# Optimization experiments

Hardware: AMD Instinct MI355X
Metric: run time of the kernel (lower is better)

The kernel has to match this reference:

```python
import jax, jax.numpy as jnp
import numpy as np

H = 8        # num_heads
D = 64       # qkv_dim
E = 512      # embed_dim = H*D
MS = 16      # ms_hidden_dim


def setup_inputs() -> dict:
    key = jax.random.key(0)
    ks = jax.random.split(key, 12)
    b, r, c = 4, 512, 512
    row_emb = jax.random.normal(ks[0], (b, r, E), dtype=jnp.float32)
    col_emb = jax.random.normal(ks[1], (b, c, E), dtype=jnp.float32)
    cost_mat = jax.random.uniform(ks[2], (b, r, c), dtype=jnp.float32)
    attn_mask = jax.random.randint(ks[3], (b, H, r, c), 0, 2) > 0
    s = 1.0 / np.sqrt(E)
    Wq = jax.random.uniform(ks[4], (H * D, E), minval=-s, maxval=s)
    Wk = jax.random.uniform(ks[5], (H * D, E), minval=-s, maxval=s)
    Wv = jax.random.uniform(ks[6], (H * D, E), minval=-s, maxval=s)
    Wout = jax.random.uniform(ks[7], (E, E), minval=-s, maxval=s)
    m1 = np.sqrt(0.5)
    m2 = np.sqrt(1.0 / MS)
    Wmix1 = jax.random.uniform(ks[8], (H * MS, 2 * H), minval=-m1, maxval=m1)
    Wmix2 = jax.random.uniform(ks[9], (H, H * MS), minval=-m2, maxval=m2)
    return {"row_emb": row_emb, "col_emb": col_emb, "cost_mat": cost_mat,
            "attn_mask": attn_mask, "Wq": Wq, "Wk": Wk, "Wv": Wv,
            "Wmix1": Wmix1, "Wmix2": Wmix2, "Wout": Wout}


def reference(row_emb, col_emb, cost_mat, attn_mask, Wq, Wk, Wv, Wmix1, Wmix2, Wout):
    b, r, _ = row_emb.shape
    c = col_emb.shape[1]
    norm = 1.0 / jnp.sqrt(jnp.asarray(D, row_emb.dtype))
    # projections -> [b, h, s, d]
    q = (row_emb @ Wq.T).reshape(b, r, H, D).transpose(0, 2, 1, 3)
    k = (col_emb @ Wk.T).reshape(b, c, H, D).transpose(0, 2, 1, 3)
    v = (col_emb @ Wv.T).reshape(b, c, H, D).transpose(0, 2, 1, 3)
    dot = norm * jnp.einsum('bhrd,bhcd->bhrc', q, k)            # [b,h,r,c]
    cost = jnp.broadcast_to(cost_mat[:, None, :, :], dot.shape)  # [b,h,r,c]
    # stack then rearrange 'b h r c s -> b r c (h s)' (h major, s minor)
    two = jnp.stack([dot, cost], axis=-1)                        # [b,h,r,c,2]
    two = two.transpose(0, 2, 3, 1, 4).reshape(b, r, c, 2 * H)
    hid = jax.nn.relu(two @ Wmix1.T)                             # [b,r,c,H*MS]
    ms = hid @ Wmix2.T                                           # [b,r,c,H]
    logits = ms.transpose(0, 3, 1, 2)                            # [b,h,r,c]
    # mask handling: rows that are fully masked become fully unmasked
    all_masked = jnp.all(attn_mask, axis=-1, keepdims=True)
    mask = jnp.where(all_masked, False, attn_mask)
    logits = jnp.where(mask, -jnp.inf, logits)
    weights = jax.nn.softmax(logits, axis=-1)
    out = jnp.einsum('bhrc,bhcd->bhrd', weights, v)              # [b,h,r,d]
    out = out.transpose(0, 2, 1, 3).reshape(b, r, H * D)         # b s (h d)
    return out @ Wout.T
```

## Files before the change

kernel.cpp:

```cpp
#include <hip/hip_runtime.h>
#include <math.h>

typedef __attribute__((ext_vector_type(8))) short bf16x8;
typedef __attribute__((ext_vector_type(4))) float f32x4;
typedef unsigned short ushort_t;

static __device__ inline unsigned short f2bf(float f) {
    union { float f; unsigned u; } v; v.f = f;
    unsigned r = v.u + 0x7fff + ((v.u >> 16) & 1);
    return (unsigned short)(r >> 16);
}

#if defined(__has_builtin)
#  if __has_builtin(__builtin_amdgcn_cvt_pk_bf16_f32)
#    define HAVE_PK_BF16 1
#  endif
#endif

static __device__ inline unsigned pk2bf(float a, float b) {
#ifdef HAVE_PK_BF16
    auto r = __builtin_amdgcn_cvt_pk_bf16_f32(a, b);
    unsigned u; __builtin_memcpy(&u, &r, 4);
    return u;
#else
    return (unsigned)f2bf(a) | ((unsigned)f2bf(b) << 16);
#endif
}

__global__ __launch_bounds__(256) void convert_all(const float* __restrict__ a0,
                                                   const float* __restrict__ a1,
                                                   const float* __restrict__ a2,
                                                   const float* __restrict__ a3,
                                                   const float* __restrict__ a4,
                                                   const float* __restrict__ a5,
                                                   ushort_t* __restrict__ dst) {
    const size_t e = ((size_t)blockIdx.x * 256 + threadIdx.x) * 4;
    const float* src; size_t off;
    if      (e < 1048576) { src = a0; off = 0; }
    else if (e < 2097152) { src = a1; off = 1048576; }
    else if (e < 2359296) { src = a2; off = 2097152; }
    else if (e < 2621440) { src = a3; off = 2359296; }
    else if (e < 2883584) { src = a4; off = 2621440; }
    else                  { src = a5; off = 2883584; }
    const float4 v = *(const float4*)(src + (e - off));
    uint2 o; o.x = pk2bf(v.x, v.y); o.y = pk2bf(v.z, v.w);
    *(uint2*)(dst + e) = o;
}

__global__ __launch_bounds__(256) void gemm_qkv(const ushort_t* __restrict__ rowb,
                                                const ushort_t* __restrict__ colb,
                                                const ushort_t* __restrict__ Wqb,
                                                const ushort_t* __restrict__ Wkb,
                                                const ushort_t* __restrict__ Wvb,
                                                ushort_t* __restrict__ Qb,
                                                ushort_t* __restrict__ Kb,
                                                ushort_t* __restrict__ Vt) {
    const int z = blockIdx.z;
    const ushort_t* A = (z == 0) ? rowb : colb;
    const ushort_t* B = (z == 0) ? Wqb : (z == 1) ? Wkb : Wvb;

    const int t    = threadIdx.x;
    const int w    = t >> 6;
    const int lane = t & 63;
    const int quad = lane >> 4;
    const int sl   = lane & 15;
    const int m0 = blockIdx.x * 64 + (w >> 1) * 32;
    const int n0 = blockIdx.y * 64 + (w & 1) * 32;

    const ushort_t* ap0 = A + (size_t)(m0 + sl) * 512 + quad * 8;
    const ushort_t* ap1 = A + (size_t)(m0 + 16 + sl) * 512 + quad * 8;
    const ushort_t* bp0 = B + (size_t)(n0 + sl) * 512 + quad * 8;
    const ushort_t* bp1 = B + (size_t)(n0 + 16 + sl) * 512 + quad * 8;

    f32x4 acc[2][2] = {};

    bf16x8 a0 = *(const bf16x8*)ap0;
    bf16x8 a1 = *(const bf16x8*)ap1;
    bf16x8 b0 = *(const bf16x8*)bp0;
    bf16x8 b1 = *(const bf16x8*)bp1;

    for (int ks = 0; ks < 16; ++ks) {
        bf16x8 na0, na1, nb0, nb1;
        if (ks < 15) {
            const int k0 = (ks + 1) * 32;
            na0 = *(const bf16x8*)(ap0 + k0);
            na1 = *(const bf16x8*)(ap1 + k0);
            nb0 = *(const bf16x8*)(bp0 + k0);
            nb1 = *(const bf16x8*)(bp1 + k0);
        }
        acc[0][0] = __builtin_amdgcn_mfma_f32_16x16x32_bf16(a0, b0, acc[0][0], 0, 0, 0);
        acc[0][1] = __builtin_amdgcn_mfma_f32_16x16x32_bf16(a0, b1, acc[0][1], 0, 0, 0);
        acc[1][0] = __builtin_amdgcn_mfma_f32_16x16x32_bf16(a1, b0, acc[1][0], 0, 0, 0);
        acc[1][1] = __builtin_amdgcn_mfma_f32_16x16x32_bf16(a1, b1, acc[1][1], 0, 0, 0);
        a0 = na0; a1 = na1; b0 = nb0; b1 = nb1;
    }

#pragma unroll
    for (int rs = 0; rs < 2; ++rs)
#pragma unroll
        for (int cs = 0; cs < 2; ++cs) {
            const int n = n0 + cs * 16 + sl;
            if (z == 2) {
                const int mb   = m0 + rs * 16 + quad * 4;
                const int bidx = mb >> 9, c = mb & 511;
                const int h = n >> 6, d = n & 63;
                ushort4 o;
                o.x = f2bf(acc[rs][cs][0]); o.y = f2bf(acc[rs][cs][1]);
                o.z = f2bf(acc[rs][cs][2]); o.w = f2bf(acc[rs][cs][3]);
                *(ushort4*)(Vt + (size_t)(((bidx * 8 + h) * 64 + d)) * 512 + c) = o;
            } else {
                ushort_t* C = (z == 0) ? Qb : Kb;
#pragma unroll
                for (int reg = 0; reg < 4; ++reg) {
                    const int m = m0 + rs * 16 + quad * 4 + reg;
                    C[(size_t)m * 512 + n] = f2bf(acc[rs][cs][reg]);
                }
            }
        }
}

__global__ __launch_bounds__(256) void gemm_out(const ushort_t* __restrict__ A,
                                                const ushort_t* __restrict__ B,
                                                float* __restrict__ C) {
    const int t    = threadIdx.x;
    const int w    = t >> 6;
    const int lane = t & 63;
    const int quad = lane >> 4;
    const int sl   = lane & 15;
    const int m0 = blockIdx.x * 64 + (w >> 1) * 32;
    const int n0 = blockIdx.y * 64 + (w & 1) * 32;

    const ushort_t* ap0 = A + (size_t)(m0 + sl) * 512 + quad * 8;
    const ushort_t* ap1 = A + (size_t)(m0 + 16 + sl) * 512 + quad * 8;
    const ushort_t* bp0 = B + (size_t)(n0 + sl) * 512 + quad * 8;
    const ushort_t* bp1 = B + (size_t)(n0 + 16 + sl) * 512 + quad * 8;

    f32x4 acc[2][2] = {};

    bf16x8 a0 = *(const bf16x8*)ap0;
    bf16x8 a1 = *(const bf16x8*)ap1;
    bf16x8 b0 = *(const bf16x8*)bp0;
    bf16x8 b1 = *(const bf16x8*)bp1;

    for (int ks = 0; ks < 16; ++ks) {
        bf16x8 na0, na1, nb0, nb1;
        if (ks < 15) {
            const int k0 = (ks + 1) * 32;
            na0 = *(const bf16x8*)(ap0 + k0);
            na1 = *(const bf16x8*)(ap1 + k0);
            nb0 = *(const bf16x8*)(bp0 + k0);
            nb1 = *(const bf16x8*)(bp1 + k0);
        }
        acc[0][0] = __builtin_amdgcn_mfma_f32_16x16x32_bf16(a0, b0, acc[0][0], 0, 0, 0);
        acc[0][1] = __builtin_amdgcn_mfma_f32_16x16x32_bf16(a0, b1, acc[0][1], 0, 0, 0);
        acc[1][0] = __builtin_amdgcn_mfma_f32_16x16x32_bf16(a1, b0, acc[1][0], 0, 0, 0);
        acc[1][1] = __builtin_amdgcn_mfma_f32_16x16x32_bf16(a1, b1, acc[1][1], 0, 0, 0);
        a0 = na0; a1 = na1; b0 = nb0; b1 = nb1;
    }

#pragma unroll
    for (int rs = 0; rs < 2; ++rs)
#pragma unroll
        for (int cs = 0; cs < 2; ++cs) {
            const int n = n0 + cs * 16 + sl;
#pragma unroll
            for (int reg = 0; reg < 4; ++reg) {
                const int m = m0 + rs * 16 + quad * 4 + reg;
                C[(size_t)m * 512 + n] = acc[rs][cs][reg];
            }
        }
}

__global__ __launch_bounds__(512) void dot_mlp_v5(const ushort_t* __restrict__ Qb,
                                                  const ushort_t* __restrict__ Kb,
                                                  const float* __restrict__ cost,
                                                  const float* __restrict__ W1,
                                                  const float* __restrict__ W2,
                                                  float* __restrict__ logits) {
    __shared__ ushort_t Xs[1024 * 18];
    __shared__ ushort_t hidS[8 * 16 * 36];
    __shared__ ushort_t W1fs[128 * 16];
    __shared__ ushort_t W2ss[8 * 128];

    const int b  = blockIdx.z;
    const int r0 = blockIdx.y * 32;
    const int c0 = blockIdx.x * 32;
    const int t    = threadIdx.x;
    const int w    = t >> 6;
    const int lane = t & 63;
    const int quad = lane >> 4;
    const int sl   = lane & 15;

    const bf16x8 zf = {0, 0, 0, 0, 0, 0, 0, 0};

    if (t < 128) {
        float s = 0.f;
#pragma unroll
        for (int h = 0; h < 8; ++h) {
            W1fs[t * 16 + h] = f2bf(W1[t * 16 + 2 * h]);
            s += W1[t * 16 + 2 * h + 1];
        }
        W1fs[t * 16 + 8] = f2bf(s);
#pragma unroll
        for (int k = 9; k < 16; ++k) W1fs[t * 16 + k] = 0;
    }
#pragma unroll
    for (int i = 0; i < 2; ++i) W2ss[t + i * 512] = f2bf(W2[t + i * 512]);

#pragma unroll
    for (int i = 0; i < 2; ++i) {
        const int cell = t + i * 512;
        const int rl = cell >> 5, cl = cell & 31;
        unsigned* base = (unsigned*)(Xs + cell * 18 + 8);
        base[0] = (unsigned)f2bf(cost[((size_t)b * 512 + r0 + rl) * 512 + c0 + cl]);
        base[1] = 0; base[2] = 0; base[3] = 0; base[4] = 0;
    }

    {
        const int hp = w & 3;
        const int h0 = hp * 2;
        const int rs = w >> 2;
        bf16x8 af[2][2], bfr[2][2][2];
#pragma unroll
        for (int hh = 0; hh < 2; ++hh)
#pragma unroll
            for (int ks = 0; ks < 2; ++ks) {
                af[hh][ks] = *(const bf16x8*)(Qb +
                    ((size_t)(b * 512 + r0 + rs * 16 + sl) * 512 + (h0 + hh) * 64 + ks * 32 + quad * 8));
#pragma unroll
                for (int cs = 0; cs < 2; ++cs)
                    bfr[hh][cs][ks] = *(const bf16x8*)(Kb +
                        ((size_t)(b * 512 + c0 + cs * 16 + sl) * 512 + (h0 + hh) * 64 + ks * 32 + quad * 8));
            }
        f32x4 dacc[2][2];
#pragma unroll
        for (int hh = 0; hh < 2; ++hh)
#pragma unroll
            for (int cs = 0; cs < 2; ++cs) {
                f32x4 acc = {0.f, 0.f, 0.f, 0.f};
                acc = __builtin_amdgcn_mfma_f32_16x16x32_bf16(af[hh][0], bfr[hh][cs][0], acc, 0, 0, 0);
                acc = __builtin_amdgcn_mfma_f32_16x16x32_bf16(af[hh][1], bfr[hh][cs][1], acc, 0, 0, 0);
                dacc[hh][cs] = acc;
            }
#pragma unroll
        for (int cs = 0; cs < 2; ++cs)
#pragma unroll
            for (int reg = 0; reg < 4; ++reg) {
                const int cell = (rs * 16 + quad * 4 + reg) * 32 + cs * 16 + sl;
                ((unsigned*)Xs)[cell * 9 + hp] =
                    pk2bf(dacc[0][cs][reg] * 0.125f, dacc[1][cs][reg] * 0.125f);
            }
    }

    __syncthreads();

    bf16x8 bw1[8];
#pragma unroll
    for (int nt = 0; nt < 8; ++nt)
        bw1[nt] = (quad < 2) ? *(const bf16x8*)&W1fs[(nt * 16 + sl) * 16 + quad * 8] : zf;
    bf16x8 bw2[4];
#pragma unroll
    for (int ks = 0; ks < 4; ++ks) {
        union { ushort_t s[8]; bf16x8 v; } tu;
#pragma unroll
        for (int i = 0; i < 8; ++i) {
            const int p  = quad * 8 + i;
            const int jc = (p >> 1) | ((p & 1) << 4);
            tu.s[i] = (sl < 8) ? W2ss[sl * 128 + ks * 32 + jc] : (ushort_t)0;
        }
        bw2[ks] = tu.v;
    }

    ushort_t* hidW = hidS + w * (16 * 36);

#pragma unroll
    for (int mt = 0; mt < 8; ++mt) {
        const int gmt = w * 8 + mt;
        const int cb  = gmt * 16;

        bf16x8 a1 = zf;
        if (quad < 2) {
            const unsigned* xr = (const unsigned*)Xs + (size_t)(cb + sl) * 9 + quad * 4;
            union { unsigned u[4]; bf16x8 v; } tmp;
            tmp.u[0] = xr[0]; tmp.u[1] = xr[1]; tmp.u[2] = xr[2]; tmp.u[3] = xr[3];
            a1 = tmp.v;
        }

        f32x4 acc2 = {0.f, 0.f, 0.f, 0.f};
#pragma unroll
        for (int ks = 0; ks < 4; ++ks) {
            f32x4 z = {0.f, 0.f, 0.f, 0.f};
            const f32x4 h0 = __builtin_amdgcn_mfma_f32_16x16x32_bf16(a1, bw1[2 * ks],     z, 0, 0, 0);
            const f32x4 h1 = __builtin_amdgcn_mfma_f32_16x16x32_bf16(a1, bw1[2 * ks + 1], z, 0, 0, 0);
#pragma unroll
            for (int rp = 0; rp < 4; ++rp)
                ((unsigned*)hidW)[(quad * 4 + rp) * 18 + sl] =
                    pk2bf(fmaxf(h0[rp], 0.f), fmaxf(h1[rp], 0.f));
            union { uint2 u2[2]; bf16x8 v; } tu;
            const ushort_t* hp2 = hidW + sl * 36 + quad * 8;
            tu.u2[0] = *(const uint2*)hp2;
            tu.u2[1] = *(const uint2*)(hp2 + 4);
            acc2 = __builtin_amdgcn_mfma_f32_16x16x32_bf16(tu.v, bw2[ks], acc2, 0, 0, 0);
        }

        if (sl < 8) {
            const int r = r0 + (gmt >> 1);
            const int cbase = c0 + (gmt & 1) * 16 + quad * 4;
            float4 o; o.x = acc2[0]; o.y = acc2[1]; o.z = acc2[2]; o.w = acc2[3];
            *(float4*)&logits[((size_t)(b * 8 + sl) * 512 + r) * 512 + cbase] = o;
        }
    }
}

__global__ __launch_bounds__(256) void softmax_pv(const float* __restrict__ logits,
                                                  const int* __restrict__ mask,
                                                  const ushort_t* __restrict__ Vt,
                                                  ushort_t* __restrict__ Aout) {
    __shared__ ushort_t Ps[16 * 520];

    const int t    = threadIdx.x;
    const int w    = t >> 6;
    const int lane = t & 63;
    const int quad = lane >> 4;
    const int sl   = lane & 15;
    const int rt = blockIdx.x;
    const int bh = blockIdx.y;
    const int r0 = rt * 16;

#pragma unroll
    for (int rr = 0; rr < 4; ++rr) {
        const int row = w * 4 + rr;
        const float* lp = logits + ((size_t)bh * 512 + r0 + row) * 512;
        const int*   mp = mask   + ((size_t)bh * 512 + r0 + row) * 512;

        float v[8]; int m[8]; int allm = 1;
#pragma unroll
        for (int i = 0; i < 8; ++i) {
            v[i] = lp[lane + i * 64];
            m[i] = mp[lane + i * 64];
            allm &= (m[i] != 0);
        }
        const bool all_masked = (__all(allm) != 0);

        float mx = -__builtin_inff();
#pragma unroll
        for (int i = 0; i < 8; ++i) {
            const bool keep = all_masked || (m[i] == 0);
            if (keep) mx = fmaxf(mx, v[i]);
        }
#pragma unroll
        for (int s = 32; s > 0; s >>= 1) mx = fmaxf(mx, __shfl_xor(mx, s, 64));

        float e[8]; float sum = 0.f;
#pragma unroll
        for (int i = 0; i < 8; ++i) {
            const bool keep = all_masked || (m[i] == 0);
            e[i] = keep ? __expf(v[i] - mx) : 0.f;
            sum += e[i];
        }
#pragma unroll
        for (int s = 32; s > 0; s >>= 1) sum += __shfl_xor(sum, s, 64);

        const float inv = 1.f / sum;
#pragma unroll
        for (int i = 0; i < 8; ++i)
            Ps[row * 520 + lane + i * 64] = f2bf(e[i] * inv);
    }

    __syncthreads();

    const int n0w = w * 16;
    const ushort_t* vb = Vt + (size_t)bh * 64 * 512;

    f32x4 acc = {0.f, 0.f, 0.f, 0.f};
    for (int ks = 0; ks < 16; ++ks) {
        union { uint2 u2[2]; bf16x8 v; } ta;
        const ushort_t* pp = Ps + (size_t)sl * 520 + ks * 32 + quad * 8;
        ta.u2[0] = *(const uint2*)pp;
        ta.u2[1] = *(const uint2*)(pp + 4);
        const bf16x8 bv = *(const bf16x8*)(vb + (size_t)(n0w + sl) * 512 + ks * 32 + quad * 8);
        acc = __builtin_amdgcn_mfma_f32_16x16x32_bf16(ta.v, bv, acc, 0, 0, 0);
    }

    const int bidx = bh >> 3, h = bh & 7;
    ushort_t* Cb = Aout + (size_t)bidx * 512 * 512 + h * 64;
    const int n = n0w + sl;
#pragma unroll
    for (int reg = 0; reg < 4; ++reg) {
        const int m = r0 + quad * 4 + reg;
        Cb[(size_t)m * 512 + n] = f2bf(acc[reg]);
    }
}

extern "C" void kernel_launch(void* const* d_in, const int* in_sizes, int n_in,
                              void* d_out, int out_size, void* d_ws, size_t ws_size,
                              hipStream_t stream) {
    const float* row_emb = (const float*)d_in[0];
    const float* col_emb = (const float*)d_in[1];
    const float* cost    = (const float*)d_in[2];
    const int*   mask    = (const int*)d_in[3];
    const float* Wq      = (const float*)d_in[4];
    const float* Wk      = (const float*)d_in[5];
    const float* Wv      = (const float*)d_in[6];
    const float* Wmix1   = (const float*)d_in[7];
    const float* Wmix2   = (const float*)d_in[8];
    const float* Wout    = (const float*)d_in[9];
    float* out = (float*)d_out;

    char* ws = (char*)d_ws;
    const size_t MB = (size_t)1 << 20;
    ushort_t* convDst = (ushort_t*)ws;
    ushort_t* rowb  = (ushort_t*)(ws);
    ushort_t* colb  = (ushort_t*)(ws + 2 * MB);
    ushort_t* Wqb   = (ushort_t*)(ws + 4 * MB);
    ushort_t* Wkb   = (ushort_t*)(ws + 4 * MB + 512 * 1024);
    ushort_t* Wvb   = (ushort_t*)(ws + 5 * MB);
    ushort_t* Woutb = (ushort_t*)(ws + 5 * MB + 512 * 1024);
    ushort_t* Qb    = (ushort_t*)(ws + 6 * MB);
    ushort_t* Kb    = (ushort_t*)(ws + 8 * MB);
    ushort_t* Vt    = (ushort_t*)(ws + 10 * MB);
    ushort_t* Aoutb = (ushort_t*)(ws + 12 * MB);
    float* logitsBuf = (float*)(ws + 16 * MB);

    convert_all<<<3072, 256, 0, stream>>>(row_emb, col_emb, Wq, Wk, Wv, Wout, convDst);

    gemm_qkv<<<dim3(32, 8, 3), 256, 0, stream>>>(rowb, colb, Wqb, Wkb, Wvb, Qb, Kb, Vt);

    dot_mlp_v5<<<dim3(16, 16, 4), 512, 0, stream>>>(Qb, Kb, cost, Wmix1, Wmix2, logitsBuf);

    softmax_pv<<<dim3(32, 32), 256, 0, stream>>>(logitsBuf, mask, Vt, Aoutb);

    gemm_out<<<dim3(32, 8), 256, 0, stream>>>(Aoutb, Woutb, out);
}
```

Baseline: 190.6 us.

## Shrink GEMM tiles with split-K accumulators, swizzle X smem, batch hidden MFMAs

The QKV and output GEMMs now use 32-row block tiles and run two independent K-half accumulator chains per wave. This doubles the grid and adds instruction-level parallelism, at the cost of reloading the B operand more often. In the dot/MLP kernel, an XOR row swizzle is applied to the Xs shared tile to cut LDS bank conflicts. All eight first-layer MFMAs are now issued before any hidden values go to a wider, padded shared buffer, which removes the per-step store/load serialization. This raises register and LDS use.

```diff
diff --git a/kernel.cpp b/kernel.cpp
--- a/kernel.cpp
+++ b/kernel.cpp
@@ -25,6 +25,10 @@
 #else
     return (unsigned)f2bf(a) | ((unsigned)f2bf(b) << 16);
 #endif
+}
+
+static __device__ inline int xrow(int cell) {
+    return cell ^ (((cell >> 7) & 1) << 4);
 }
 
 __global__ __launch_bounds__(256) void convert_all(const float* __restrict__ a0,
@@ -64,59 +68,58 @@
     const int lane = t & 63;
     const int quad = lane >> 4;
     const int sl   = lane & 15;
-    const int m0 = blockIdx.x * 64 + (w >> 1) * 32;
+    const int m0 = blockIdx.x * 32 + (w >> 1) * 16;
     const int n0 = blockIdx.y * 64 + (w & 1) * 32;
 
-    const ushort_t* ap0 = A + (size_t)(m0 + sl) * 512 + quad * 8;
-    const ushort_t* ap1 = A + (size_t)(m0 + 16 + sl) * 512 + quad * 8;
+    const ushort_t* ap  = A + (size_t)(m0 + sl) * 512 + quad * 8;
     const ushort_t* bp0 = B + (size_t)(n0 + sl) * 512 + quad * 8;
     const ushort_t* bp1 = B + (size_t)(n0 + 16 + sl) * 512 + quad * 8;
 
-    f32x4 acc[2][2] = {};
-
-    bf16x8 a0 = *(const bf16x8*)ap0;
-    bf16x8 a1 = *(const bf16x8*)ap1;
-    bf16x8 b0 = *(const bf16x8*)bp0;
-    bf16x8 b1 = *(const bf16x8*)bp1;
-
-    for (int ks = 0; ks < 16; ++ks) {
-        bf16x8 na0, na1, nb0, nb1;
-        if (ks < 15) {
-            const int k0 = (ks + 1) * 32;
-            na0 = *(const bf16x8*)(ap0 + k0);
-            na1 = *(const bf16x8*)(ap1 + k0);
-            nb0 = *(const bf16x8*)(bp0 + k0);
-            nb1 = *(const bf16x8*)(bp1 + k0);
-        }
-        acc[0][0] = __builtin_amdgcn_mfma_f32_16x16x32_bf16(a0, b0, acc[0][0], 0, 0, 0);
-        acc[0][1] = __builtin_amdgcn_mfma_f32_16x16x32_bf16(a0, b1, acc[0][1], 0, 0, 0);
-        acc[1][0] = __builtin_amdgcn_mfma_f32_16x16x32_bf16(a1, b0, acc[1][0], 0, 0, 0);
-        acc[1][1] = __builtin_amdgcn_mfma_f32_16x16x32_bf16(a1, b1, acc[1][1], 0, 0, 0);
-        a0 = na0; a1 = na1; b0 = nb0; b1 = nb1;
-    }
-
-#pragma unroll
-    for (int rs = 0; rs < 2; ++rs)
-#pragma unroll
-        for (int cs = 0; cs < 2; ++cs) {
-            const int n = n0 + cs * 16 + sl;
-            if (z == 2) {
-                const int mb   = m0 + rs * 16 + quad * 4;
-                const int bidx = mb >> 9, c = mb & 511;
-                const int h = n >> 6, d = n & 63;
-                ushort4 o;
-                o.x = f2bf(acc[rs][cs][0]); o.y = f2bf(acc[rs][cs][1]);
-                o.z = f2bf(acc[rs][cs][2]); o.w = f2bf(acc[rs][cs][3]);
-                *(ushort4*)(Vt + (size_t)(((bidx * 8 + h) * 64 + d)) * 512 + c) = o;
-            } else {
-                ushort_t* C = (z == 0) ? Qb : Kb;
-#pragma unroll
-                for (int reg = 0; reg < 4; ++reg) {
-                    const int m = m0 + rs * 16 + quad * 4 + reg;
-                    C[(size_t)m * 512 + n] = f2bf(acc[rs][cs][reg]);
-                }
+    f32x4 accA[2] = {}, accB[2] = {};
+
+    bf16x8 aA = *(const bf16x8*)ap,          b0A = *(const bf16x8*)bp0,
+           b1A = *(const bf16x8*)bp1;
+    bf16x8 aB = *(const bf16x8*)(ap + 256),  b0B = *(const bf16x8*)(bp0 + 256),
+           b1B = *(const bf16x8*)(bp1 + 256);
+
+    for (int ks = 0; ks < 8; ++ks) {
+        bf16x8 naA, nb0A, nb1A, naB, nb0B, nb1B;
+        if (ks < 7) {
+            const int o = (ks + 1) * 32;
+            naA  = *(const bf16x8*)(ap + o);        nb0A = *(const bf16x8*)(bp0 + o);
+            nb1A = *(const bf16x8*)(bp1 + o);
+            naB  = *(const bf16x8*)(ap + 256 + o);  nb0B = *(const bf16x8*)(bp0 + 256 + o);
+            nb1B = *(const bf16x8*)(bp1 + 256 + o);
+        }
+        accA[0] = __builtin_amdgcn_mfma_f32_16x16x32_bf16(aA, b0A, accA[0], 0, 0, 0);
+        accA[1] = __builtin_amdgcn_mfma_f32_16x16x32_bf16(aA, b1A, accA[1], 0, 0, 0);
+        accB[0] = __builtin_amdgcn_mfma_f32_16x16x32_bf16(aB, b0B, accB[0], 0, 0, 0);
+        accB[1] = __builtin_amdgcn_mfma_f32_16x16x32_bf16(aB, b1B, accB[1], 0, 0, 0);
+        aA = naA; b0A = nb0A; b1A = nb1A;
+        aB = naB; b0B = nb0B; b1B = nb1B;
+    }
+
+#pragma unroll
+    for (int cs = 0; cs < 2; ++cs) {
+        const f32x4 acc = accA[cs] + accB[cs];
+        const int n = n0 + cs * 16 + sl;
+        if (z == 2) {
+            const int mb   = m0 + quad * 4;
+            const int bidx = mb >> 9, c = mb & 511;
+            const int h = n >> 6, d = n & 63;
+            ushort4 o;
+            o.x = f2bf(acc[0]); o.y = f2bf(acc[1]);
+            o.z = f2bf(acc[2]); o.w = f2bf(acc[3]);
+            *(ushort4*)(Vt + (size_t)(((bidx * 8 + h) * 64 + d)) * 512 + c) = o;
+        } else {
+            ushort_t* C = (z == 0) ? Qb : Kb;
+#pragma unroll
+            for (int reg = 0; reg < 4; ++reg) {
+                const int m = m0 + quad * 4 + reg;
+                C[(size_t)m * 512 + n] = f2bf(acc[reg]);
             }
         }
+    }
 }
 
 __global__ __launch_bounds__(256) void gemm_out(const ushort_t* __restrict__ A,
@@ -127,58 +130,57 @@
     const int lane = t & 63;
     const int quad = lane >> 4;
     const int sl   = lane & 15;
-    const int m0 = blockIdx.x * 64 + (w >> 1) * 32;
+    const int m0 = blockIdx.x * 32 + (w >> 1) * 16;
     const int n0 = blockIdx.y * 64 + (w & 1) * 32;
 
-    const ushort_t* ap0 = A + (size_t)(m0 + sl) * 512 + quad * 8;
-    const ushort_t* ap1 = A + (size_t)(m0 + 16 + sl) * 512 + quad * 8;
+    const ushort_t* ap  = A + (size_t)(m0 + sl) * 512 + quad * 8;
     const ushort_t* bp0 = B + (size_t)(n0 + sl) * 512 + quad * 8;
     const ushort_t* bp1 = B + (size_t)(n0 + 16 + sl) * 512 + quad * 8;
 
-    f32x4 acc[2][2] = {};
-
-    bf16x8 a0 = *(const bf16x8*)ap0;
-    bf16x8 a1 = *(const bf16x8*)ap1;
-    bf16x8 b0 = *(const bf16x8*)bp0;
-    bf16x8 b1 = *(const bf16x8*)bp1;
-
-    for (int ks = 0; ks < 16; ++ks) {
-        bf16x8 na0, na1, nb0, nb1;
-        if (ks < 15) {
-            const int k0 = (ks + 1) * 32;
-            na0 = *(const bf16x8*)(ap0 + k0);
-            na1 = *(const bf16x8*)(ap1 + k0);
-            nb0 = *(const bf16x8*)(bp0 + k0);
-            nb1 = *(const bf16x8*)(bp1 + k0);
-        }
-        acc[0][0] = __builtin_amdgcn_mfma_f32_16x16x32_bf16(a0, b0, acc[0][0], 0, 0, 0);
-        acc[0][1] = __builtin_amdgcn_mfma_f32_16x16x32_bf16(a0, b1, acc[0][1], 0, 0, 0);
-        acc[1][0] = __builtin_amdgcn_mfma_f32_16x16x32_bf16(a1, b0, acc[1][0], 0, 0, 0);
-        acc[1][1] = __builtin_amdgcn_mfma_f32_16x16x32_bf16(a1, b1, acc[1][1], 0, 0, 0);
-        a0 = na0; a1 = na1; b0 = nb0; b1 = nb1;
-    }
-
-#pragma unroll
-    for (int rs = 0; rs < 2; ++rs)
-#pragma unroll
-        for (int cs = 0; cs < 2; ++cs) {
-            const int n = n0 + cs * 16 + sl;
-#pragma unroll
-            for (int reg = 0; reg < 4; ++reg) {
-                const int m = m0 + rs * 16 + quad * 4 + reg;
-                C[(size_t)m * 512 + n] = acc[rs][cs][reg];
-            }
-        }
-}
-
-__global__ __launch_bounds__(512) void dot_mlp_v5(const ushort_t* __restrict__ Qb,
+    f32x4 accA[2] = {}, accB[2] = {};
+
+    bf16x8 aA = *(const bf16x8*)ap,          b0A = *(const bf16x8*)bp0,
+           b1A = *(const bf16x8*)bp1;
+    bf16x8 aB = *(const bf16x8*)(ap + 256),  b0B = *(const bf16x8*)(bp0 + 256),
+           b1B = *(const bf16x8*)(bp1 + 256);
+
+    for (int ks = 0; ks < 8; ++ks) {
+        bf16x8 naA, nb0A, nb1A, naB, nb0B, nb1B;
+        if (ks < 7) {
+            const int o = (ks + 1) * 32;
+            naA  = *(const bf16x8*)(ap + o);        nb0A = *(const bf16x8*)(bp0 + o);
+            nb1A = *(const bf16x8*)(bp1 + o);
+            naB  = *(const bf16x8*)(ap + 256 + o);  nb0B = *(const bf16x8*)(bp0 + 256 + o);
+            nb1B = *(const bf16x8*)(bp1 + 256 + o);
+        }
+        accA[0] = __builtin_amdgcn_mfma_f32_16x16x32_bf16(aA, b0A, accA[0], 0, 0, 0);
+        accA[1] = __builtin_amdgcn_mfma_f32_16x16x32_bf16(aA, b1A, accA[1], 0, 0, 0);
+        accB[0] = __builtin_amdgcn_mfma_f32_16x16x32_bf16(aB, b0B, accB[0], 0, 0, 0);
+        accB[1] = __builtin_amdgcn_mfma_f32_16x16x32_bf16(aB, b1B, accB[1], 0, 0, 0);
+        aA = naA; b0A = nb0A; b1A = nb1A;
+        aB = naB; b0B = nb0B; b1B = nb1B;
+    }
+
+#pragma unroll
+    for (int cs = 0; cs < 2; ++cs) {
+        const f32x4 acc = accA[cs] + accB[cs];
+        const int n = n0 + cs * 16 + sl;
+#pragma unroll
+        for (int reg = 0; reg < 4; ++reg) {
+            const int m = m0 + quad * 4 + reg;
+            C[(size_t)m * 512 + n] = acc[reg];
+        }
+    }
+}
+
+__global__ __launch_bounds__(512) void dot_mlp_v6(const ushort_t* __restrict__ Qb,
                                                   const ushort_t* __restrict__ Kb,
                                                   const float* __restrict__ cost,
                                                   const float* __restrict__ W1,
                                                   const float* __restrict__ W2,
                                                   float* __restrict__ logits) {
     __shared__ ushort_t Xs[1024 * 18];
-    __shared__ ushort_t hidS[8 * 16 * 36];
+    __shared__ unsigned hidU[8 * 16 * 65];
     __shared__ ushort_t W1fs[128 * 16];
     __shared__ ushort_t W2ss[8 * 128];
 
@@ -211,7 +213,7 @@
     for (int i = 0; i < 2; ++i) {
         const int cell = t + i * 512;
         const int rl = cell >> 5, cl = cell & 31;
-        unsigned* base = (unsigned*)(Xs + cell * 18 + 8);
+        unsigned* base = (unsigned*)(Xs + xrow(cell) * 18 + 8);
         base[0] = (unsigned)f2bf(cost[((size_t)b * 512 + r0 + rl) * 512 + c0 + cl]);
         base[1] = 0; base[2] = 0; base[3] = 0; base[4] = 0;
     }
@@ -247,7 +249,7 @@
 #pragma unroll
             for (int reg = 0; reg < 4; ++reg) {
                 const int cell = (rs * 16 + quad * 4 + reg) * 32 + cs * 16 + sl;
-                ((unsigned*)Xs)[cell * 9 + hp] =
+                ((unsigned*)Xs)[xrow(cell) * 9 + hp] =
                     pk2bf(dacc[0][cs][reg] * 0.125f, dacc[1][cs][reg] * 0.125f);
             }
     }
@@ -271,7 +273,7 @@
         bw2[ks] = tu.v;
     }
 
-    ushort_t* hidW = hidS + w * (16 * 36);
+    unsigned* hidW = hidU + w * (16 * 65);
 
 #pragma unroll
     for (int mt = 0; mt < 8; ++mt) {
@@ -280,26 +282,31 @@
 
         bf16x8 a1 = zf;
         if (quad < 2) {
-            const unsigned* xr = (const unsigned*)Xs + (size_t)(cb + sl) * 9 + quad * 4;
+            const unsigned* xr = (const unsigned*)Xs + (size_t)xrow(cb + sl) * 9 + quad * 4;
             union { unsigned u[4]; bf16x8 v; } tmp;
             tmp.u[0] = xr[0]; tmp.u[1] = xr[1]; tmp.u[2] = xr[2]; tmp.u[3] = xr[3];
             a1 = tmp.v;
         }
 
+        f32x4 hacc[8];
+#pragma unroll
+        for (int nt = 0; nt < 8; ++nt) {
+            f32x4 z = {0.f, 0.f, 0.f, 0.f};
+            hacc[nt] = __builtin_amdgcn_mfma_f32_16x16x32_bf16(a1, bw1[nt], z, 0, 0, 0);
+        }
+#pragma unroll
+        for (int g = 0; g < 4; ++g)
+#pragma unroll
+            for (int rp = 0; rp < 4; ++rp)
+                hidW[(quad * 4 + rp) * 65 + g * 16 + sl] =
+                    pk2bf(fmaxf(hacc[2 * g][rp], 0.f), fmaxf(hacc[2 * g + 1][rp], 0.f));
+
         f32x4 acc2 = {0.f, 0.f, 0.f, 0.f};
 #pragma unroll
         for (int ks = 0; ks < 4; ++ks) {
-            f32x4 z = {0.f, 0.f, 0.f, 0.f};
-            const f32x4 h0 = __builtin_amdgcn_mfma_f32_16x16x32_bf16(a1, bw1[2 * ks],     z, 0, 0, 0);
-            const f32x4 h1 = __builtin_amdgcn_mfma_f32_16x16x32_bf16(a1, bw1[2 * ks + 1], z, 0, 0, 0);
-#pragma unroll
-            for (int rp = 0; rp < 4; ++rp)
-                ((unsigned*)hidW)[(quad * 4 + rp) * 18 + sl] =
-                    pk2bf(fmaxf(h0[rp], 0.f), fmaxf(h1[rp], 0.f));
-            union { uint2 u2[2]; bf16x8 v; } tu;
-            const ushort_t* hp2 = hidW + sl * 36 + quad * 8;
-            tu.u2[0] = *(const uint2*)hp2;
-            tu.u2[1] = *(const uint2*)(hp2 + 4);
+            union { unsigned u[4]; bf16x8 v; } tu;
+            const unsigned* hp2 = hidW + sl * 65 + ks * 16 + quad * 4;
+            tu.u[0] = hp2[0]; tu.u[1] = hp2[1]; tu.u[2] = hp2[2]; tu.u[3] = hp2[3];
             acc2 = __builtin_amdgcn_mfma_f32_16x16x32_bf16(tu.v, bw2[ks], acc2, 0, 0, 0);
         }
 
@@ -424,11 +431,11 @@
 
     convert_all<<<3072, 256, 0, stream>>>(row_emb, col_emb, Wq, Wk, Wv, Wout, convDst);
 
-    gemm_qkv<<<dim3(32, 8, 3), 256, 0, stream>>>(rowb, colb, Wqb, Wkb, Wvb, Qb, Kb, Vt);
-
-    dot_mlp_v5<<<dim3(16, 16, 4), 512, 0, stream>>>(Qb, Kb, cost, Wmix1, Wmix2, logitsBuf);
+    gemm_qkv<<<dim3(64, 8, 3), 256, 0, stream>>>(rowb, colb, Wqb, Wkb, Wvb, Qb, Kb, Vt);
+
+    dot_mlp_v6<<<dim3(16, 16, 4), 512, 0, stream>>>(Qb, Kb, cost, Wmix1, Wmix2, logitsBuf);
 
     softmax_pv<<<dim3(32, 32), 256, 0, stream>>>(logitsBuf, mask, Vt, Aoutb);
 
-    gemm_out<<<dim3(32, 8), 256, 0, stream>>>(Aoutb, Woutb, out);
-}
+    gemm_out<<<dim3(64, 8), 256, 0, stream>>>(Aoutb, Woutb, out);
+}
```

Result: slower. 209.6 us (+10.0%).
